# Performance work log

Hardware: AMD Instinct MI355X
Metric: run time of the kernel (lower is better)

## Reference

```python
import jax, jax.numpy as jnp
import numpy as np

B, S, HID = 2, 1024, 4096
NQ, NG, D = 32, 4, 128
NKV = NQ // NG  # 8 kv heads
OFF = 1024


def setup_inputs() -> dict:
    key = jax.random.key(0)
    ks = jax.random.split(key, 13)
    w = 0.02
    return {
        "x": jax.random.normal(ks[0], (B, S, HID), jnp.float32),
        "offset": OFF,
        "precomp_freqs_cos": jax.random.uniform(ks[1], (S, D // 2), jnp.float32, -1.0, 1.0),
        "precomp_freqs_sin": jax.random.uniform(ks[2], (S, D // 2), jnp.float32, -1.0, 1.0),
        "k_cache": jax.random.normal(ks[3], (B, OFF, NQ, D), jnp.float32),
        "v_cache": jax.random.normal(ks[4], (B, OFF, NQ, D), jnp.float32),
        "q_w": jax.random.normal(ks[5], (NQ * D, HID), jnp.float32) * w,
        "q_b": jax.random.normal(ks[6], (NQ * D,), jnp.float32) * w,
        "k_w": jax.random.normal(ks[7], (NKV * D, HID), jnp.float32) * w,
        "k_b": jax.random.normal(ks[8], (NKV * D,), jnp.float32) * w,
        "v_w": jax.random.normal(ks[9], (NKV * D, HID), jnp.float32) * w,
        "v_b": jax.random.normal(ks[10], (NKV * D,), jnp.float32) * w,
        "o_w": jax.random.normal(ks[11], (HID, NQ * D), jnp.float32) * w,
    }


def _rope(x, cos, sin):
    # x: [b, s, h, d]; cos/sin: [s, d//2] applied to interleaved pairs
    b, s, h, d = x.shape
    xp = x.reshape(b, s, h, d // 2, 2)
    xr, xi = xp[..., 0], xp[..., 1]
    c = cos[None, :, None, :]
    sn = sin[None, :, None, :]
    out = jnp.stack([xr * c - xi * sn, xr * sn + xi * c], axis=-1)
    return out.reshape(b, s, h, d)


def reference(x, offset, precomp_freqs_cos, precomp_freqs_sin, k_cache, v_cache,
              q_w, q_b, k_w, k_b, v_w, v_b, o_w):
    b, s, _ = x.shape
    q = (x @ q_w.T + q_b).reshape(b, s, NQ, D)
    k = (x @ k_w.T + k_b).reshape(b, s, NKV, D)
    v = (x @ v_w.T + v_b).reshape(b, s, NKV, D)
    # GQA expansion: '(hr)' -> each kv head repeated NG times contiguously
    k = jnp.repeat(k, NG, axis=2)  # [b, s, NQ, D]
    v = jnp.repeat(v, NG, axis=2)
    q = _rope(q, precomp_freqs_cos, precomp_freqs_sin)
    k = _rope(k, precomp_freqs_cos, precomp_freqs_sin)
    k = jnp.concatenate([k_cache, k], axis=1)  # [b, offset+s, NQ, D]
    v = jnp.concatenate([v_cache, v], axis=1)
    qk = jnp.einsum('bsnd,btnd->bnst', q, k) / np.float32(np.sqrt(D))
    neg_inf = jnp.asarray(-jnp.inf, qk.dtype)
    causal = jnp.triu(jnp.full((s, s), neg_inf, qk.dtype), k=1)
    mask = jnp.concatenate([jnp.zeros((s, offset), qk.dtype), causal], axis=1)
    qk = qk + mask[None, None, :, :]
    p = jax.nn.softmax(qk, axis=-1)
    out = jnp.einsum('bnst,btnd->bsnd', p, v).reshape(b, s, NQ * D)
    out = out @ o_w.T
    return (out, k, v)
```

## Files before the change

kernel.cpp:

```cpp
#include <hip/hip_runtime.h>
#include <hip/hip_bf16.h>
#include <cstdio>
#include <cstdint>

typedef __bf16 bf16_t;
typedef __bf16 bf16x8 __attribute__((ext_vector_type(8)));
typedef float f32x4 __attribute__((ext_vector_type(4)));

static constexpr int Bc = 2, Sc = 1024, HIDc = 4096;
static constexpr int NQc = 32, NKVc = 8, Dc = 128, OFFc = 1024, Tc = 2048;
static constexpr int Mrows = Bc * Sc;
static constexpr int NQKV = (NQc + 2 * NKVc) * Dc;

__device__ inline void load_lds16(const void* g, void* l) {
    __builtin_amdgcn_global_load_lds(
        (const __attribute__((address_space(1))) unsigned*)g,
        (__attribute__((address_space(3))) unsigned*)l, 16, 0, 0);
}

__global__ void k_cvt(const float* __restrict__ src, bf16_t* __restrict__ dst, long n4) {
    long i = blockIdx.x * (long)blockDim.x + threadIdx.x;
    long stride = (long)gridDim.x * blockDim.x;
    const float4* s4 = (const float4*)src;
    for (; i < n4; i += stride) {
        float4 v = s4[i];
        bf16_t t[4] = {(bf16_t)v.x, (bf16_t)v.y, (bf16_t)v.z, (bf16_t)v.w};
        *(uint2*)&dst[i * 4] = *(uint2*)t;
    }
}

template <bool BIAS, bool OUT_BF16>
__global__ __launch_bounds__(256) void k_gemm(const bf16_t* __restrict__ A,
                                              const bf16_t* __restrict__ Bm,
                                              const float* __restrict__ bias,
                                              void* __restrict__ Cout,
                                              int M, int N, int K) {
    __shared__ __align__(16) bf16_t As[128][32];
    __shared__ __align__(16) bf16_t Bs[128][32];
    const int tid = threadIdx.x, wid = tid >> 6, lane = tid & 63;
    const int g = lane >> 4, ln = lane & 15;
    const int wm = wid >> 1, wn = wid & 1;
    const int gx = gridDim.x;
    int bidl = blockIdx.y * gx + blockIdx.x;
    int cpx = (gx * gridDim.y) >> 3;
    int swz = (bidl & 7) * cpx + (bidl >> 3);
    const int m0 = (swz / gx) * 128, n0 = (swz % gx) * 128;
    f32x4 acc[4][4] = {};

    for (int k0 = 0; k0 < K; k0 += 32) {
        __syncthreads();
#pragma unroll
        for (int c = 0; c < 2; ++c) {
            int row = wid * 32 + c * 16 + (lane >> 2);
            int col = (lane & 3) * 8;
            load_lds16(A + (size_t)(m0 + row) * K + k0 + col, &As[wid * 32 + c * 16][0]);
            load_lds16(Bm + (size_t)(n0 + row) * K + k0 + col, &Bs[wid * 32 + c * 16][0]);
        }
        __syncthreads();
        bf16x8 af[4], bfr[4];
#pragma unroll
        for (int i = 0; i < 4; ++i) af[i] = *(const bf16x8*)&As[wm * 64 + i * 16 + ln][g * 8];
#pragma unroll
        for (int i = 0; i < 4; ++i) bfr[i] = *(const bf16x8*)&Bs[wn * 64 + i * 16 + ln][g * 8];
#pragma unroll
        for (int i = 0; i < 4; ++i)
#pragma unroll
            for (int j = 0; j < 4; ++j)
                acc[i][j] = __builtin_amdgcn_mfma_f32_16x16x32_bf16(af[i], bfr[j], acc[i][j], 0, 0, 0);
    }

#pragma unroll
    for (int i = 0; i < 4; ++i) {
#pragma unroll
        for (int j = 0; j < 4; ++j) {
            int col = n0 + wn * 64 + j * 16 + ln;
            float bv = BIAS ? bias[col] : 0.f;
#pragma unroll
            for (int r = 0; r < 4; ++r) {
                int row = m0 + wm * 64 + i * 16 + g * 4 + r;
                float v = acc[i][j][r] + bv;
                if (OUT_BF16)
                    ((bf16_t*)Cout)[(size_t)row * N + col] = (bf16_t)v;
                else
                    ((float*)Cout)[(size_t)row * N + col] = v;
            }
        }
    }
}

__global__ void k_rope_q(bf16_t* __restrict__ qkv, const float* __restrict__ cosT,
                         const float* __restrict__ sinT) {
    int row = blockIdx.x;
    int s = row & 1023;
    bf16_t* src = qkv + (size_t)row * NQKV;
    for (int p = threadIdx.x; p < 2048; p += 256) {
        int j = p & 63;
        float c = cosT[s * 64 + j], sn = sinT[s * 64 + j];
        float xr = (float)src[2 * p], xi = (float)src[2 * p + 1];
        src[2 * p]     = (bf16_t)(xr * c - xi * sn);
        src[2 * p + 1] = (bf16_t)(xr * sn + xi * c);
    }
}


__global__ __launch_bounds__(256) void k_ropekv(const bf16_t* __restrict__ qkv,
                                                const float* __restrict__ cosT,
                                                const float* __restrict__ sinT,
                                                float* __restrict__ out_k,
                                                float* __restrict__ out_v,
                                                bf16_t* __restrict__ kfr,
                                                bf16_t* __restrict__ vfr) {
    __shared__ __align__(16) bf16_t Vl[64][136];
    const int sb = blockIdx.x, hk = blockIdx.y, b = blockIdx.z;
    const int tid = threadIdx.x;
    const int tt = tid >> 2, dq = (tid & 3) * 32;
    const int s = sb * 64 + tt;
    const int t = OFFc + s;
    const bf16_t* krow = qkv + (size_t)(b * Sc + s) * NQKV + NQc * Dc + hk * Dc + dq;
    const bf16_t* vrow = qkv + (size_t)(b * Sc + s) * NQKV + (NQc + NKVc) * Dc + hk * Dc + dq;

    float cs[16], sn[16];
    int j0 = dq >> 1;
#pragma unroll
    for (int q4 = 0; q4 < 4; ++q4) {
        float4 cv = *(const float4*)&cosT[s * 64 + j0 + q4 * 4];
        float4 sv = *(const float4*)&sinT[s * 64 + j0 + q4 * 4];
        cs[q4 * 4] = cv.x; cs[q4 * 4 + 1] = cv.y; cs[q4 * 4 + 2] = cv.z; cs[q4 * 4 + 3] = cv.w;
        sn[q4 * 4] = sv.x; sn[q4 * 4 + 1] = sv.y; sn[q4 * 4 + 2] = sv.z; sn[q4 * 4 + 3] = sv.w;
    }

    bf16_t kb[32], vb[32];
#pragma unroll
    for (int c = 0; c < 4; ++c) {
        *(uint4*)&kb[c * 8] = *(const uint4*)&krow[c * 8];
        *(uint4*)&vb[c * 8] = *(const uint4*)&vrow[c * 8];
    }
    float ko[32], vo[32];
    bf16_t kbf[32];
#pragma unroll
    for (int jj = 0; jj < 16; ++jj) {
        float xr = (float)kb[2 * jj], xi = (float)kb[2 * jj + 1];
        ko[2 * jj]     = xr * cs[jj] - xi * sn[jj];
        ko[2 * jj + 1] = xr * sn[jj] + xi * cs[jj];
        kbf[2 * jj]     = (bf16_t)ko[2 * jj];
        kbf[2 * jj + 1] = (bf16_t)ko[2 * jj + 1];
        vo[2 * jj] = (float)vb[2 * jj];
        vo[2 * jj + 1] = (float)vb[2 * jj + 1];
    }

    const int t16 = t >> 4, lnr = t & 15, dc = dq >> 5;
#pragma unroll
    for (int gg = 0; gg < 4; ++gg) {
        int hq = hk * 4 + gg;
        size_t o = ((size_t)(b * Tc + t) * NQc + hq) * Dc + dq;
#pragma unroll
        for (int c = 0; c < 8; ++c) {
            *(float4*)&out_k[o + c * 4] = *(float4*)&ko[c * 4];
            *(float4*)&out_v[o + c * 4] = *(float4*)&vo[c * 4];
        }
        size_t fb = ((size_t)b * NQc + hq) * ((size_t)Tc * Dc);
#pragma unroll
        for (int g = 0; g < 4; ++g)
            *(uint4*)&kfr[fb + (size_t)(((t16 * 4 + dc) * 4 + g) * 128 + lnr * 8)] = *(uint4*)&kbf[g * 8];
    }
#pragma unroll
    for (int c = 0; c < 4; ++c) *(uint4*)&Vl[tt][dq + c * 8] = *(uint4*)&vb[c * 8];
    __syncthreads();
    const int tile = 16 + sb;
#pragma unroll
    for (int i = 0; i < 4; ++i) {
        int u = i * 256 + tid;
        int d = u >> 3, cc = u & 7;
        bf16_t tmp[8];
#pragma unroll
        for (int j = 0; j < 8; ++j) tmp[j] = Vl[cc * 8 + j][d];
        size_t off = (size_t)((((tile * 8 + (d >> 4)) * 2 + (cc >> 2)) * 4 + (cc & 3)) * 128 + (d & 15) * 8);
#pragma unroll
        for (int gg = 0; gg < 4; ++gg) {
            int hq = hk * 4 + gg;
            size_t fb = ((size_t)b * NQc + hq) * ((size_t)Tc * Dc);
            *(uint4*)&vfr[fb + off] = *(uint4*)tmp;
        }
    }
}

__global__ __launch_bounds__(256) void k_cache(const float* __restrict__ kc,
                                               const float* __restrict__ vc,
                                               float* __restrict__ out_k,
                                               float* __restrict__ out_v,
                                               bf16_t* __restrict__ kfr,
                                               bf16_t* __restrict__ vfr) {
    __shared__ __align__(16) bf16_t Vl[64][136];
    const int tb = blockIdx.x, h = blockIdx.y, b = blockIdx.z;
    const int tid = threadIdx.x;
    const int tt = tid >> 2, dq = (tid & 3) * 32;
    const int t = tb * 64 + tt;
    size_t src = ((size_t)(b * OFFc + t) * NQc + h) * Dc + dq;
    size_t dst = ((size_t)(b * Tc + t) * NQc + h) * Dc + dq;
    const size_t fb = ((size_t)b * NQc + h) * ((size_t)Tc * Dc);

    bf16_t kb[32], vb[32];
#pragma unroll
    for (int c = 0; c < 8; ++c) {
        float4 kv = *(const float4*)&kc[src + c * 4];
        *(float4*)&out_k[dst + c * 4] = kv;
        kb[c * 4] = (bf16_t)kv.x; kb[c * 4 + 1] = (bf16_t)kv.y;
        kb[c * 4 + 2] = (bf16_t)kv.z; kb[c * 4 + 3] = (bf16_t)kv.w;
        float4 vv = *(const float4*)&vc[src + c * 4];
        *(float4*)&out_v[dst + c * 4] = vv;
        vb[c * 4] = (bf16_t)vv.x; vb[c * 4 + 1] = (bf16_t)vv.y;
        vb[c * 4 + 2] = (bf16_t)vv.z; vb[c * 4 + 3] = (bf16_t)vv.w;
    }
    const int t16 = t >> 4, lnr = t & 15, dc = dq >> 5;
#pragma unroll
    for (int g = 0; g < 4; ++g)
        *(uint4*)&kfr[fb + (size_t)(((t16 * 4 + dc) * 4 + g) * 128 + lnr * 8)] = *(uint4*)&kb[g * 8];

#pragma unroll
    for (int c = 0; c < 4; ++c) *(uint4*)&Vl[tt][dq + c * 8] = *(uint4*)&vb[c * 8];
    __syncthreads();
#pragma unroll
    for (int i = 0; i < 4; ++i) {
        int u = i * 256 + tid;
        int d = u >> 3, cc = u & 7;
        bf16_t tmp[8];
#pragma unroll
        for (int j = 0; j < 8; ++j) tmp[j] = Vl[cc * 8 + j][d];
        size_t off = (size_t)((((tb * 8 + (d >> 4)) * 2 + (cc >> 2)) * 4 + (cc & 3)) * 128 + (d & 15) * 8);
        *(uint4*)&vfr[fb + off] = *(uint4*)tmp;
    }
}

__global__ __launch_bounds__(512) void k_attn(const bf16_t* __restrict__ qkv,
                                              const bf16_t* __restrict__ kfr,
                                              const bf16_t* __restrict__ vfr,
                                              bf16_t* __restrict__ attn) {
    __shared__ __align__(16) bf16_t Kl[2][8192];
    __shared__ __align__(16) bf16_t Vl2[2][8192];
    __shared__ __align__(16) bf16_t Pl[8][2048];
    const int tid = threadIdx.x, w = tid >> 6, l = tid & 63;
    const int g = l >> 4, ln = l & 15;
    const int bid = blockIdx.x;
    const int xcd = bid & 7, within = bid >> 3;
    const int qblk = 3 - (within & 3);
    const int u = within >> 2;
    const int b = u >> 2;
    const int h = (u & 3) * 8 + xcd;
    const int q0b = qblk * 256;
    const int qw0 = q0b + w * 32;
    const float SCALE = 0.08838834764831845f;
    const float L2E = 1.4426950408889634f;
    const size_t hb = ((size_t)b * NQc + h) * ((size_t)Tc * Dc);
    const bf16_t* kb = kfr + hb;
    const bf16_t* vb = vfr + hb;
    bf16_t* Pw = &Pl[w][0];

    bf16x8 qf[2][4];
#pragma unroll
    for (int mf = 0; mf < 2; ++mf) {
        size_t qrow = (size_t)(b * Sc + qw0 + mf * 16 + ln) * NQKV + h * Dc;
#pragma unroll
        for (int dc = 0; dc < 4; ++dc) qf[mf][dc] = *(const bf16x8*)&qkv[qrow + dc * 32 + g * 8];
    }
    f32x4 o[2][8] = {};
    float mrun[2][4], lrun[2][4];
#pragma unroll
    for (int mf = 0; mf < 2; ++mf)
#pragma unroll
        for (int r = 0; r < 4; ++r) { mrun[mf][r] = -1e30f; lrun[mf][r] = 0.f; }

    const int ntiles = (OFFc + q0b + 256) >> 6;

    auto stage = [&](int bf, int t) {
        const bf16_t* ksrc = kb + (size_t)t * 8192 + (size_t)(w * 2) * 512;
        const bf16_t* vsrc = vb + (size_t)t * 8192 + (size_t)(w * 2) * 512;
        load_lds16(ksrc + (size_t)l * 8,       &Kl[bf][(w * 2) * 512]);
        load_lds16(ksrc + 512 + (size_t)l * 8, &Kl[bf][(w * 2 + 1) * 512]);
        load_lds16(vsrc + (size_t)l * 8,       &Vl2[bf][(w * 2) * 512]);
        load_lds16(vsrc + 512 + (size_t)l * 8, &Vl2[bf][(w * 2 + 1) * 512]);
    };

    stage(0, 0);
    __syncthreads();
    int cur = 0;

    for (int t = 0; t < ntiles; ++t) {
        if (t + 1 < ntiles) stage(cur ^ 1, t + 1);
        f32x4 sa[2][4] = {};
#pragma unroll
        for (int nf = 0; nf < 4; ++nf) {
            bf16x8 kf[4];
#pragma unroll
            for (int dc = 0; dc < 4; ++dc)
                kf[dc] = *(const bf16x8*)&Kl[cur][((nf * 4 + dc) * 4 + g) * 128 + ln * 8];
#pragma unroll
            for (int dc = 0; dc < 4; ++dc) {
                sa[0][nf] = __builtin_amdgcn_mfma_f32_16x16x32_bf16(qf[0][dc], kf[dc], sa[0][nf], 0, 0, 0);
                sa[1][nf] = __builtin_amdgcn_mfma_f32_16x16x32_bf16(qf[1][dc], kf[dc], sa[1][nf], 0, 0, 0);
            }
        }
        bool maybe = (t * 64 + 63 > OFFc + qw0);
#pragma unroll
        for (int mf = 0; mf < 2; ++mf)
#pragma unroll
            for (int nf = 0; nf < 4; ++nf)
#pragma unroll
                for (int r = 0; r < 4; ++r) {
                    float s = sa[mf][nf][r] * SCALE;
                    if (maybe) {
                        int tg = t * 64 + nf * 16 + ln;
                        int qg = qw0 + mf * 16 + g * 4 + r;
                        if (tg > OFFc + qg) s = -1e30f;
                    }
                    sa[mf][nf][r] = s;
                }
        float tm[2][4];
        int grew = 0;
#pragma unroll
        for (int mf = 0; mf < 2; ++mf)
#pragma unroll
            for (int r = 0; r < 4; ++r) {
                float m2 = fmaxf(fmaxf(sa[mf][0][r], sa[mf][1][r]), fmaxf(sa[mf][2][r], sa[mf][3][r]));
#pragma unroll
                for (int msk = 1; msk < 16; msk <<= 1) m2 = fmaxf(m2, __shfl_xor(m2, msk));
                tm[mf][r] = m2;
                grew |= (m2 > mrun[mf][r]) ? 1 : 0;
            }
        if (__any(grew)) {
#pragma unroll
            for (int mf = 0; mf < 2; ++mf) {
                float al[4];
#pragma unroll
                for (int r = 0; r < 4; ++r) {
                    float mn = fmaxf(mrun[mf][r], tm[mf][r]);
                    al[r] = exp2f((mrun[mf][r] - mn) * L2E);
                    mrun[mf][r] = mn;
                    lrun[mf][r] *= al[r];
                }
#pragma unroll
                for (int df = 0; df < 8; ++df) {
                    f32x4 t4 = o[mf][df];
                    t4[0] *= al[0]; t4[1] *= al[1]; t4[2] *= al[2]; t4[3] *= al[3];
                    o[mf][df] = t4;
                }
            }
        }
        float ps[2][4] = {};
#pragma unroll
        for (int mf = 0; mf < 2; ++mf)
#pragma unroll
            for (int nf = 0; nf < 4; ++nf)
#pragma unroll
                for (int r = 0; r < 4; ++r) {
                    float p = exp2f((sa[mf][nf][r] - mrun[mf][r]) * L2E);
                    ps[mf][r] += p;
                    int q = mf * 16 + g * 4 + r;
                    int k = nf * 16 + ln;
                    Pw[q * 64 + (((k >> 3) ^ (q & 7)) << 3) + (k & 7)] = (bf16_t)p;
                }
#pragma unroll
        for (int mf = 0; mf < 2; ++mf)
#pragma unroll
            for (int r = 0; r < 4; ++r) {
                float s2 = ps[mf][r];
#pragma unroll
                for (int msk = 1; msk < 16; msk <<= 1) s2 += __shfl_xor(s2, msk);
                lrun[mf][r] += s2;
            }
#pragma unroll
        for (int kc = 0; kc < 2; ++kc) {
            bf16x8 vf[8];
#pragma unroll
            for (int df = 0; df < 8; ++df)
                vf[df] = *(const bf16x8*)&Vl2[cur][((df * 2 + kc) * 4 + g) * 128 + ln * 8];
#pragma unroll
            for (int mf = 0; mf < 2; ++mf) {
                bf16x8 pa = *(const bf16x8*)&Pw[(mf * 16 + ln) * 64 + (((kc * 4 + g) ^ (ln & 7)) << 3)];
#pragma unroll
                for (int df = 0; df < 8; ++df)
                    o[mf][df] = __builtin_amdgcn_mfma_f32_16x16x32_bf16(pa, vf[df], o[mf][df], 0, 0, 0);
            }
        }
        __syncthreads();
        cur ^= 1;
    }

#pragma unroll
    for (int mf = 0; mf < 2; ++mf)
#pragma unroll
        for (int df = 0; df < 8; ++df)
#pragma unroll
            for (int r = 0; r < 4; ++r) {
                float v = o[mf][df][r] / lrun[mf][r];
                size_t orow = (size_t)(b * Sc + qw0 + mf * 16 + g * 4 + r) * (NQc * Dc) + h * Dc + df * 16 + ln;
                attn[orow] = (bf16_t)v;
            }
}

extern "C" void kernel_launch(void* const* d_in, const int* in_sizes, int n_in,
                              void* d_out, int out_size, void* d_ws, size_t ws_size,
                              hipStream_t stream) {
    const float* x      = (const float*)d_in[0];
    const float* cosT   = (const float*)d_in[2];
    const float* sinT   = (const float*)d_in[3];
    const float* kcache = (const float*)d_in[4];
    const float* vcache = (const float*)d_in[5];
    const float* q_w    = (const float*)d_in[6];
    const float* q_b    = (const float*)d_in[7];
    const float* k_w    = (const float*)d_in[8];
    const float* k_b    = (const float*)d_in[9];
    const float* v_w    = (const float*)d_in[10];
    const float* v_b    = (const float*)d_in[11];
    const float* o_w    = (const float*)d_in[12];

    char* ws = (char*)d_ws;
    size_t off = 0;
    auto alloc = [&](size_t bytes) {
        void* p = ws + off;
        off += (bytes + 255) & ~(size_t)255;
        return p;
    };
    bf16_t* xb   = (bf16_t*)alloc((size_t)Mrows * HIDc * 2);
    bf16_t* wqkv = (bf16_t*)alloc((size_t)Bc * Tc * NQc * Dc * 4);
    bf16_t* owb  = (bf16_t*)alloc((size_t)HIDc * HIDc * 2);
    bf16_t* qkv  = (bf16_t*)alloc((size_t)Mrows * NQKV * 2);
    float*  bias = (float*)alloc((size_t)NQKV * 4);
    if (off > ws_size) {
        fprintf(stderr, "WS too small: need %zu have %zu\n", off, ws_size);
        return;
    }
    bf16_t* attn  = xb;
    bf16_t* kfr = wqkv;
    bf16_t* vfr = wqkv + (size_t)Bc * NQc * Tc * Dc;

    float* out_o = (float*)d_out;
    float* out_k = out_o + (size_t)Mrows * HIDc;
    float* out_v = out_k + (size_t)Bc * Tc * NQc * Dc;

    k_cvt<<<2048, 256, 0, stream>>>(x, xb, (long)Mrows * HIDc / 4);
    k_cvt<<<2048, 256, 0, stream>>>(q_w, wqkv, (long)NQc * Dc * HIDc / 4);
    k_cvt<<<1024, 256, 0, stream>>>(k_w, wqkv + (size_t)NQc * Dc * HIDc, (long)NKVc * Dc * HIDc / 4);
    k_cvt<<<1024, 256, 0, stream>>>(v_w, wqkv + (size_t)(NQc + NKVc) * Dc * HIDc, (long)NKVc * Dc * HIDc / 4);
    k_cvt<<<2048, 256, 0, stream>>>(o_w, owb, (long)HIDc * HIDc / 4);
    (void)hipMemcpyAsync(bias, q_b, (size_t)NQc * Dc * 4, hipMemcpyDeviceToDevice, stream);
    (void)hipMemcpyAsync(bias + NQc * Dc, k_b, (size_t)NKVc * Dc * 4, hipMemcpyDeviceToDevice, stream);
    (void)hipMemcpyAsync(bias + (NQc + NKVc) * Dc, v_b, (size_t)NKVc * Dc * 4, hipMemcpyDeviceToDevice, stream);

    k_gemm<true, true><<<dim3(NQKV / 128, Mrows / 128), 256, 0, stream>>>(
        xb, wqkv, bias, qkv, Mrows, NQKV, HIDc);
    k_rope_q<<<Mrows, 256, 0, stream>>>(qkv, cosT, sinT);
    k_ropekv<<<dim3(16, 8, 2), 256, 0, stream>>>(qkv, cosT, sinT, out_k, out_v, kfr, vfr);
    k_cache<<<dim3(16, 32, 2), 256, 0, stream>>>(kcache, vcache, out_k, out_v, kfr, vfr);
    k_attn<<<256, 512, 0, stream>>>(qkv, kfr, vfr, attn);
    k_gemm<false, false><<<dim3(HIDc / 128, Mrows / 128), 256, 0, stream>>>(
        attn, owb, nullptr, d_out, Mrows, HIDc, HIDc);
}
```

Baseline: 559.5 us.

## Split attention into 128-row query blocks and transpose QK^T MFMA layout

```diff
diff --git a/kernel.cpp b/kernel.cpp
--- a/kernel.cpp
+++ b/kernel.cpp
@@ -231,22 +231,22 @@
     }
 }
 
-__global__ __launch_bounds__(512) void k_attn(const bf16_t* __restrict__ qkv,
+__global__ __launch_bounds__(256) void k_attn(const bf16_t* __restrict__ qkv,
                                               const bf16_t* __restrict__ kfr,
                                               const bf16_t* __restrict__ vfr,
                                               bf16_t* __restrict__ attn) {
     __shared__ __align__(16) bf16_t Kl[2][8192];
     __shared__ __align__(16) bf16_t Vl2[2][8192];
-    __shared__ __align__(16) bf16_t Pl[8][2048];
+    __shared__ __align__(16) bf16_t Pl[4][2048];
     const int tid = threadIdx.x, w = tid >> 6, l = tid & 63;
     const int g = l >> 4, ln = l & 15;
     const int bid = blockIdx.x;
     const int xcd = bid & 7, within = bid >> 3;
-    const int qblk = 3 - (within & 3);
-    const int u = within >> 2;
+    const int qblk = 7 - (within & 7);
+    const int u = within >> 3;
     const int b = u >> 2;
     const int h = (u & 3) * 8 + xcd;
-    const int q0b = qblk * 256;
+    const int q0b = qblk * 128;
     const int qw0 = q0b + w * 32;
     const float SCALE = 0.08838834764831845f;
     const float L2E = 1.4426950408889634f;
@@ -263,21 +263,21 @@
         for (int dc = 0; dc < 4; ++dc) qf[mf][dc] = *(const bf16x8*)&qkv[qrow + dc * 32 + g * 8];
     }
     f32x4 o[2][8] = {};
-    float mrun[2][4], lrun[2][4];
-#pragma unroll
-    for (int mf = 0; mf < 2; ++mf)
-#pragma unroll
-        for (int r = 0; r < 4; ++r) { mrun[mf][r] = -1e30f; lrun[mf][r] = 0.f; }
-
-    const int ntiles = (OFFc + q0b + 256) >> 6;
+    float mrun[2] = {-1e30f, -1e30f};
+    float lrun[2] = {0.f, 0.f};
+
+    const int ntiles = (OFFc + q0b + 128) >> 6;
 
     auto stage = [&](int bf, int t) {
-        const bf16_t* ksrc = kb + (size_t)t * 8192 + (size_t)(w * 2) * 512;
-        const bf16_t* vsrc = vb + (size_t)t * 8192 + (size_t)(w * 2) * 512;
-        load_lds16(ksrc + (size_t)l * 8,       &Kl[bf][(w * 2) * 512]);
-        load_lds16(ksrc + 512 + (size_t)l * 8, &Kl[bf][(w * 2 + 1) * 512]);
-        load_lds16(vsrc + (size_t)l * 8,       &Vl2[bf][(w * 2) * 512]);
-        load_lds16(vsrc + 512 + (size_t)l * 8, &Vl2[bf][(w * 2 + 1) * 512]);
+        const bf16_t* ksrc = kb + (size_t)t * 8192;
+        const bf16_t* vsrc = vb + (size_t)t * 8192;
+#pragma unroll
+        for (int c = 0; c < 4; ++c) {
+            int off = (c * 256 + tid) * 8;
+            int base = (c * 256 + (tid & ~63)) * 8;
+            load_lds16(ksrc + off, &Kl[bf][base]);
+            load_lds16(vsrc + off, &Vl2[bf][base]);
+        }
     };
 
     stage(0, 0);
@@ -295,8 +295,8 @@
                 kf[dc] = *(const bf16x8*)&Kl[cur][((nf * 4 + dc) * 4 + g) * 128 + ln * 8];
 #pragma unroll
             for (int dc = 0; dc < 4; ++dc) {
-                sa[0][nf] = __builtin_amdgcn_mfma_f32_16x16x32_bf16(qf[0][dc], kf[dc], sa[0][nf], 0, 0, 0);
-                sa[1][nf] = __builtin_amdgcn_mfma_f32_16x16x32_bf16(qf[1][dc], kf[dc], sa[1][nf], 0, 0, 0);
+                sa[0][nf] = __builtin_amdgcn_mfma_f32_16x16x32_bf16(kf[dc], qf[0][dc], sa[0][nf], 0, 0, 0);
+                sa[1][nf] = __builtin_amdgcn_mfma_f32_16x16x32_bf16(kf[dc], qf[1][dc], sa[1][nf], 0, 0, 0);
             }
         }
         bool maybe = (t * 64 + 63 > OFFc + qw0);
@@ -308,65 +308,65 @@
                 for (int r = 0; r < 4; ++r) {
                     float s = sa[mf][nf][r] * SCALE;
                     if (maybe) {
-                        int tg = t * 64 + nf * 16 + ln;
-                        int qg = qw0 + mf * 16 + g * 4 + r;
+                        int tg = t * 64 + nf * 16 + g * 4 + r;
+                        int qg = qw0 + mf * 16 + ln;
                         if (tg > OFFc + qg) s = -1e30f;
                     }
                     sa[mf][nf][r] = s;
                 }
-        float tm[2][4];
+        float tm[2];
         int grew = 0;
 #pragma unroll
-        for (int mf = 0; mf < 2; ++mf)
-#pragma unroll
-            for (int r = 0; r < 4; ++r) {
-                float m2 = fmaxf(fmaxf(sa[mf][0][r], sa[mf][1][r]), fmaxf(sa[mf][2][r], sa[mf][3][r]));
-#pragma unroll
-                for (int msk = 1; msk < 16; msk <<= 1) m2 = fmaxf(m2, __shfl_xor(m2, msk));
-                tm[mf][r] = m2;
-                grew |= (m2 > mrun[mf][r]) ? 1 : 0;
-            }
+        for (int mf = 0; mf < 2; ++mf) {
+            float m2 = sa[mf][0][0];
+#pragma unroll
+            for (int nf = 0; nf < 4; ++nf)
+#pragma unroll
+                for (int r = 0; r < 4; ++r) m2 = fmaxf(m2, sa[mf][nf][r]);
+            m2 = fmaxf(m2, __shfl_xor(m2, 16));
+            m2 = fmaxf(m2, __shfl_xor(m2, 32));
+            tm[mf] = m2;
+            grew |= (m2 > mrun[mf]) ? 1 : 0;
+        }
         if (__any(grew)) {
 #pragma unroll
             for (int mf = 0; mf < 2; ++mf) {
-                float al[4];
-#pragma unroll
-                for (int r = 0; r < 4; ++r) {
-                    float mn = fmaxf(mrun[mf][r], tm[mf][r]);
-                    al[r] = exp2f((mrun[mf][r] - mn) * L2E);
-                    mrun[mf][r] = mn;
-                    lrun[mf][r] *= al[r];
-                }
+                float mn = fmaxf(mrun[mf], tm[mf]);
+                float al = exp2f((mrun[mf] - mn) * L2E);
+                mrun[mf] = mn;
+                lrun[mf] *= al;
+                float alr[4];
+#pragma unroll
+                for (int r = 0; r < 4; ++r)
+                    alr[r] = __shfl(al, (l & 48) | (g * 4 + r));
 #pragma unroll
                 for (int df = 0; df < 8; ++df) {
                     f32x4 t4 = o[mf][df];
-                    t4[0] *= al[0]; t4[1] *= al[1]; t4[2] *= al[2]; t4[3] *= al[3];
+                    t4[0] *= alr[0]; t4[1] *= alr[1]; t4[2] *= alr[2]; t4[3] *= alr[3];
                     o[mf][df] = t4;
                 }
             }
         }
-        float ps[2][4] = {};
-#pragma unroll
-        for (int mf = 0; mf < 2; ++mf)
-#pragma unroll
-            for (int nf = 0; nf < 4; ++nf)
+#pragma unroll
+        for (int mf = 0; mf < 2; ++mf) {
+            const int qrow = mf * 16 + ln;
+            float ps = 0.f;
+#pragma unroll
+            for (int nf = 0; nf < 4; ++nf) {
+                bf16_t pv[4];
 #pragma unroll
                 for (int r = 0; r < 4; ++r) {
-                    float p = exp2f((sa[mf][nf][r] - mrun[mf][r]) * L2E);
-                    ps[mf][r] += p;
-                    int q = mf * 16 + g * 4 + r;
-                    int k = nf * 16 + ln;
-                    Pw[q * 64 + (((k >> 3) ^ (q & 7)) << 3) + (k & 7)] = (bf16_t)p;
+                    float p = exp2f((sa[mf][nf][r] - mrun[mf]) * L2E);
+                    ps += p;
+                    pv[r] = (bf16_t)p;
                 }
-#pragma unroll
-        for (int mf = 0; mf < 2; ++mf)
-#pragma unroll
-            for (int r = 0; r < 4; ++r) {
-                float s2 = ps[mf][r];
-#pragma unroll
-                for (int msk = 1; msk < 16; msk <<= 1) s2 += __shfl_xor(s2, msk);
-                lrun[mf][r] += s2;
-            }
+                int slot = (nf * 2 + (g >> 1)) ^ (ln & 7);
+                *(uint2*)&Pw[qrow * 64 + slot * 8 + (g & 1) * 4] = *(uint2*)pv;
+            }
+            ps += __shfl_xor(ps, 16);
+            ps += __shfl_xor(ps, 32);
+            lrun[mf] += ps;
+        }
 #pragma unroll
         for (int kc = 0; kc < 2; ++kc) {
             bf16x8 vf[8];
@@ -386,15 +386,20 @@
     }
 
 #pragma unroll
-    for (int mf = 0; mf < 2; ++mf)
+    for (int mf = 0; mf < 2; ++mf) {
+        float linv[4];
+#pragma unroll
+        for (int r = 0; r < 4; ++r)
+            linv[r] = 1.f / __shfl(lrun[mf], (l & 48) | (g * 4 + r));
 #pragma unroll
         for (int df = 0; df < 8; ++df)
 #pragma unroll
             for (int r = 0; r < 4; ++r) {
-                float v = o[mf][df][r] / lrun[mf][r];
+                float v = o[mf][df][r] * linv[r];
                 size_t orow = (size_t)(b * Sc + qw0 + mf * 16 + g * 4 + r) * (NQc * Dc) + h * Dc + df * 16 + ln;
                 attn[orow] = (bf16_t)v;
             }
+    }
 }
 
 extern "C" void kernel_launch(void* const* d_in, const int* in_sizes, int n_in,
@@ -451,7 +456,7 @@
     k_rope_q<<<Mrows, 256, 0, stream>>>(qkv, cosT, sinT);
     k_ropekv<<<dim3(16, 8, 2), 256, 0, stream>>>(qkv, cosT, sinT, out_k, out_v, kfr, vfr);
     k_cache<<<dim3(16, 32, 2), 256, 0, stream>>>(kcache, vcache, out_k, out_v, kfr, vfr);
-    k_attn<<<256, 512, 0, stream>>>(qkv, kfr, vfr, attn);
+    k_attn<<<512, 256, 0, stream>>>(qkv, kfr, vfr, attn);
     k_gemm<false, false><<<dim3(HIDc / 128, Mrows / 128), 256, 0, stream>>>(
         attn, owb, nullptr, d_out, Mrows, HIDc, HIDc);
 }
```

New measurement: 607.7 us. 1.09x slower.
